# Performance work log

Hardware: AMD Instinct MI355X
Metric: run time of the kernel (lower is better)

Reference implementation:

```python
import jax, jax.numpy as jnp
import numpy as np

K = 5          # kernel_size
PAD = (K - 1) // 2  # fixed_padding with dilation=1, stride=1 -> 'same'


def setup_inputs() -> dict:
    key = jax.random.key(0)
    kx, kw = jax.random.split(key)
    x = jax.random.normal(kx, (4, 8, 512, 512), dtype=jnp.float32)
    # nn.Parameter initialized to zeros in the original; use small random values
    # so the op is non-trivial (math is identical for any weight values).
    weight = jax.random.normal(kw, (8, 8, K, K), dtype=jnp.float32) * 0.05
    return {"x": x, "weight": weight}


def reference(x, weight):
    """Morphological dilation2d with hard max (soft_max=False).

    out[n,o,h,w] = max_{c,dy,dx} ( x_pad[n,c,h+dy,w+dx] + weight[o,c,dy,dx] )
    Faithful to: pad zeros -> unfold -> weight + x -> max over dim C*k*k.
    Computed as a fused sliding-window max-plus reduction (no (N,C,k,k,H,W)
    unfold tensor is materialized; loop is over the fixed k*k kernel taps).
    """
    N, C, H, W = x.shape
    O = weight.shape[0]
    xp = jnp.pad(x, ((0, 0), (0, 0), (PAD, PAD), (PAD, PAD)))  # zero pad, as in F.pad
    out = jnp.full((N, O, H, W), -jnp.inf, dtype=x.dtype)
    for dy in range(K):
        for dx in range(K):
            patch = xp[:, :, dy:dy + H, dx:dx + W]           # (N,C,H,W)
            w_tap = weight[:, :, dy, dx]                      # (O,C)
            # (N,1,C,H,W) + (1,O,C,1,1) -> max over C -> (N,O,H,W)
            term = patch[:, None] + w_tap[None, :, :, None, None]
            out = jnp.maximum(out, jnp.max(term, axis=2))
    return out
```

## Files before the change

### kernel.cpp

```cpp
#include <hip/hip_runtime.h>
#include <math.h>
#include <stdint.h>

#define KK 5
#define PADK 2
#define C_IN 8
#define O_OUT 8
#define HH 512
#define WW 512
#define TH 8
#define TW 128
#define CH 4
#define LROWS 12
#define LCOLS 136
#define WCH 56
#define NW (O_OUT * C_IN * KK * KK)
#define XHALF (CH * LROWS * (LCOLS / 2))

static __device__ __forceinline__ float max3f(float a, float b, float c) {
    float d;
    asm("v_max3_f32 %0, %1, %2, %3" : "=v"(d) : "v"(a), "v"(b), "v"(c));
    return d;
}

__global__ __launch_bounds__(512, 4)
void dil_kernel(const float* __restrict__ x,
                const float* __restrict__ wf,
                float* __restrict__ out) {
    __shared__ __align__(16) float xlds[CH][LROWS][LCOLS];
    __shared__ __align__(16) float wlds[C_IN * 4 * WCH];

    const int tid = threadIdx.x;
    const int w0 = blockIdx.x * TW;
    const int h0 = blockIdx.y * TH;
    const int n  = blockIdx.z;
    const float* xn = x + (size_t)n * (C_IN * HH * WW);

    const int l   = tid & 63;
    const int wid = tid >> 6;
    const int og  = wid & 3;
    const int rq  = wid >> 2;
    const int rbase = rq * 4;

    float acc[2][4][2];
    #pragma unroll
    for (int a = 0; a < 2; ++a)
        #pragma unroll
        for (int j = 0; j < 4; ++j) {
            acc[a][j][0] = -INFINITY;
            acc[a][j][1] = -INFINITY;
        }

    for (int h = 0; h < 2; ++h) {
        if (h) __syncthreads();

        for (int idx = tid; idx < XHALF; idx += 512) {
            int cc  = idx / (LROWS * (LCOLS / 2));
            int rem = idx - cc * (LROWS * (LCOLS / 2));
            int r   = rem / (LCOLS / 2);
            int jp  = rem - r * (LCOLS / 2);
            int gh = h0 - PADK + r;
            int gw = w0 - PADK + 2 * jp;
            float v0 = 0.f, v1 = 0.f;
            if ((unsigned)gh < (unsigned)HH) {
                const float* row = xn + ((size_t)(h * CH + cc) * HH + gh) * WW;
                if ((unsigned)gw < (unsigned)WW) v0 = row[gw];
                if ((unsigned)(gw + 1) < (unsigned)WW) v1 = row[gw + 1];
            }
            *(float2*)&xlds[cc][r][2 * jp] = make_float2(v0, v1);
        }
        if (h == 0) {
            for (int t = tid; t < NW; t += 512) {
                int dx = t % KK;  int q = t / KK;
                int dy = q % KK;  q /= KK;
                int c  = q % C_IN;
                int o  = q / C_IN;
                int g  = o >> 1, o2 = o & 1;
                wlds[(c * 4 + g) * WCH + dy * 10 + o2 * KK + dx] = wf[t];
            }
        }
        __syncthreads();

        for (int cc = 0; cc < CH; ++cc) {
            const int c = h * CH + cc;

            float U[8][6];
            #pragma unroll
            for (int r = 0; r < 8; ++r) {
                const float* lr = &xlds[cc][rbase + r][2 * l];
                float2 a = *(const float2*)(lr);
                float2 b = *(const float2*)(lr + 2);
                float2 d = *(const float2*)(lr + 4);
                U[r][0] = a.x; U[r][1] = a.y;
                U[r][2] = b.x; U[r][3] = b.y;
                U[r][4] = d.x; U[r][5] = d.y;
            }
            float W[50];
            {
                const float* wc = &wlds[(c * 4 + og) * WCH];
                #pragma unroll
                for (int k = 0; k < 12; ++k) {
                    float4 v = *(const float4*)(wc + 4 * k);
                    W[4 * k + 0] = v.x; W[4 * k + 1] = v.y;
                    W[4 * k + 2] = v.z; W[4 * k + 3] = v.w;
                }
                float2 v = *(const float2*)(wc + 48);
                W[48] = v.x; W[49] = v.y;
            }

            #pragma unroll
            for (int dy = 0; dy < KK; ++dy) {
                #pragma unroll
                for (int j = 0; j < 4; ++j) {
                    const float u0 = U[dy + j][0], u1 = U[dy + j][1],
                                u2 = U[dy + j][2], u3 = U[dy + j][3],
                                u4 = U[dy + j][4], u5 = U[dy + j][5];
                    #pragma unroll
                    for (int o2 = 0; o2 < 2; ++o2) {
                        const int wb = dy * 10 + o2 * KK;
                        float t0 = u0 + W[wb + 0], t1 = u1 + W[wb + 1],
                              t2 = u2 + W[wb + 2], t3 = u3 + W[wb + 3],
                              t4 = u4 + W[wb + 4];
                        acc[o2][j][0] = max3f(acc[o2][j][0],
                                              max3f(t0, t1, t2),
                                              fmaxf(t3, t4));
                        float s0 = u1 + W[wb + 0], s1 = u2 + W[wb + 1],
                              s2 = u3 + W[wb + 2], s3 = u4 + W[wb + 3],
                              s4 = u5 + W[wb + 4];
                        acc[o2][j][1] = max3f(acc[o2][j][1],
                                              max3f(s0, s1, s2),
                                              fmaxf(s3, s4));
                    }
                }
            }
        }
    }

    float* onp = out + (size_t)n * (O_OUT * HH * WW);
    const int hB = h0 + rbase;
    const int wcol = w0 + 2 * l;
    #pragma unroll
    for (int o2 = 0; o2 < 2; ++o2) {
        const int o = og * 2 + o2;
        #pragma unroll
        for (int j = 0; j < 4; ++j) {
            float2 rr = make_float2(acc[o2][j][0], acc[o2][j][1]);
            *(float2*)(&onp[((size_t)o * HH + hB + j) * WW + wcol]) = rr;
        }
    }
}

extern "C" void kernel_launch(void* const* d_in, const int* in_sizes, int n_in,
                              void* d_out, int out_size, void* d_ws, size_t ws_size,
                              hipStream_t stream) {
    const float* x   = (const float*)d_in[0];
    const float* wgt = (const float*)d_in[1];
    float* out = (float*)d_out;

    dim3 grid(WW / TW, HH / TH, 4);
    dim3 block(512);
    dil_kernel<<<grid, block, 0, stream>>>(x, wgt, out);
}
```

Baseline: 70.73 us.

## Load weights as wave-uniform scalars from pre-permuted workspace instead of LDS

Adds a small prep kernel that permutes the weights into a contiguous per-output-group workspace. The main kernel then reads the weights directly from global memory with wave-uniform indices, so they can become scalar loads, and drops the weight LDS buffer and its fill loop. It also staggers the channel order per output group to spread LDS bank traffic, and raises the launch-bounds occupancy hint from 4 to 6. The cost is an extra kernel launch, possible scalar-register pressure, and tighter VGPR limits from the higher occupancy target.

```diff
diff --git a/kernel.cpp b/kernel.cpp
--- a/kernel.cpp
+++ b/kernel.cpp
@@ -13,7 +13,7 @@
 #define CH 4
 #define LROWS 12
 #define LCOLS 136
-#define WCH 56
+#define WCHUNK 64
 #define NW (O_OUT * C_IN * KK * KK)
 #define XHALF (CH * LROWS * (LCOLS / 2))
 
@@ -23,12 +23,26 @@
     return d;
 }
 
-__global__ __launch_bounds__(512, 4)
+__global__ void prep_weights_kernel(const float* __restrict__ w,
+                                    float* __restrict__ ws) {
+    int i = blockIdx.x * 256 + threadIdx.x;
+    if (i < NW) {
+        int dx = i % KK;  int q = i / KK;
+        int dy = q % KK;  q /= KK;
+        int c  = q % C_IN;
+        int o  = q / C_IN;
+        int og = o >> 1, o2 = o & 1;
+        ws[(og * C_IN + c) * WCHUNK + dy * 10 + o2 * KK + dx] = w[i];
+    }
+}
+
+template <bool USE_WS>
+__global__ __launch_bounds__(512, 6)
 void dil_kernel(const float* __restrict__ x,
                 const float* __restrict__ wf,
+                const float* __restrict__ ws,
                 float* __restrict__ out) {
     __shared__ __align__(16) float xlds[CH][LROWS][LCOLS];
-    __shared__ __align__(16) float wlds[C_IN * 4 * WCH];
 
     const int tid = threadIdx.x;
     const int w0 = blockIdx.x * TW;
@@ -37,9 +51,8 @@
     const float* xn = x + (size_t)n * (C_IN * HH * WW);
 
     const int l   = tid & 63;
-    const int wid = tid >> 6;
-    const int og  = wid & 3;
-    const int rq  = wid >> 2;
+    const int og  = __builtin_amdgcn_readfirstlane((tid >> 6) & 3);
+    const int rq  = __builtin_amdgcn_readfirstlane(tid >> 8);
     const int rbase = rq * 4;
 
     float acc[2][4][2];
@@ -69,43 +82,38 @@
             }
             *(float2*)&xlds[cc][r][2 * jp] = make_float2(v0, v1);
         }
-        if (h == 0) {
-            for (int t = tid; t < NW; t += 512) {
-                int dx = t % KK;  int q = t / KK;
-                int dy = q % KK;  q /= KK;
-                int c  = q % C_IN;
-                int o  = q / C_IN;
-                int g  = o >> 1, o2 = o & 1;
-                wlds[(c * 4 + g) * WCH + dy * 10 + o2 * KK + dx] = wf[t];
-            }
-        }
         __syncthreads();
 
-        for (int cc = 0; cc < CH; ++cc) {
-            const int c = h * CH + cc;
+        for (int ci = 0; ci < CH; ++ci) {
+            const int cl = (ci + og) & 3;
+            const int c  = h * CH + cl;
+
+            float W[50];
+            if (USE_WS) {
+                const float* wb = ws + (og * C_IN + c) * WCHUNK;
+                #pragma unroll
+                for (int k = 0; k < 50; ++k) W[k] = wb[k];
+            } else {
+                #pragma unroll
+                for (int o2 = 0; o2 < 2; ++o2)
+                    #pragma unroll
+                    for (int dy = 0; dy < KK; ++dy)
+                        #pragma unroll
+                        for (int dx = 0; dx < KK; ++dx)
+                            W[dy * 10 + o2 * KK + dx] =
+                                wf[(((og * 2 + o2) * C_IN + c) * KK + dy) * KK + dx];
+            }
 
             float U[8][6];
             #pragma unroll
             for (int r = 0; r < 8; ++r) {
-                const float* lr = &xlds[cc][rbase + r][2 * l];
+                const float* lr = &xlds[cl][rbase + r][2 * l];
                 float2 a = *(const float2*)(lr);
                 float2 b = *(const float2*)(lr + 2);
                 float2 d = *(const float2*)(lr + 4);
                 U[r][0] = a.x; U[r][1] = a.y;
                 U[r][2] = b.x; U[r][3] = b.y;
                 U[r][4] = d.x; U[r][5] = d.y;
-            }
-            float W[50];
-            {
-                const float* wc = &wlds[(c * 4 + og) * WCH];
-                #pragma unroll
-                for (int k = 0; k < 12; ++k) {
-                    float4 v = *(const float4*)(wc + 4 * k);
-                    W[4 * k + 0] = v.x; W[4 * k + 1] = v.y;
-                    W[4 * k + 2] = v.z; W[4 * k + 3] = v.w;
-                }
-                float2 v = *(const float2*)(wc + 48);
-                W[48] = v.x; W[49] = v.y;
             }
 
             #pragma unroll
@@ -159,5 +167,12 @@
 
     dim3 grid(WW / TW, HH / TH, 4);
     dim3 block(512);
-    dil_kernel<<<grid, block, 0, stream>>>(x, wgt, out);
+
+    if (ws_size >= (size_t)(4 * C_IN * WCHUNK) * sizeof(float)) {
+        float* ws = (float*)d_ws;
+        prep_weights_kernel<<<(NW + 255) / 256, 256, 0, stream>>>(wgt, ws);
+        dil_kernel<true><<<grid, block, 0, stream>>>(x, wgt, ws, out);
+    } else {
+        dil_kernel<false><<<grid, block, 0, stream>>>(x, wgt, nullptr, out);
+    }
 }
```

New measurement: 73.67 us. 4.2% more time.
